# Performance work log

Measured on AMD Instinct MI355X. Metric: run time of the kernel, lower is better.

## Reference

```python
import jax, jax.numpy as jnp
import numpy as np


def _to_complex(t):
    # last dim 2 = (real, imag) -> complex64
    return jax.lax.complex(t[..., 0], t[..., 1])


def setup_inputs() -> dict:
    key = jax.random.key(0)
    k1, k2, k3, k4 = jax.random.split(key, 4)
    N, C_out, C_in, H, Wf = 2, 64, 3, 256, 129  # Wf = 256//2 + 1 (rfft width)
    X = jax.random.normal(k1, (N, 1, C_in, H, Wf, 2), dtype=jnp.float32)
    D = jax.random.normal(k2, (N, C_out, C_in, H, Wf, 2), dtype=jnp.float32)
    Y = jax.random.normal(k3, (N, C_out, 1, H, Wf, 2), dtype=jnp.float32)
    # alpha is a positive penalty weight; offset away from 0 to avoid blow-up in Z/alpha
    alpha = jax.random.uniform(k4, (N, 1, 1, 1), dtype=jnp.float32) + 0.5
    x_size = np.array([256, 256], dtype=np.int64)  # spatial size for irfft2
    return {"X": X, "D": D, "Y": Y, "alpha": alpha, "x_size": x_size}


def reference(X, D, Y, alpha, x_size):
    C_in = X.shape[2]
    Xc = _to_complex(X)  # (N,1,C_in,H,Wf)
    Dc = _to_complex(D)  # (N,C_out,C_in,H,Wf)
    Yc = _to_complex(Y)  # (N,C_out,1,H,Wf)
    # alpha.unsqueeze(-1).unsqueeze(-1)/C_in: in complex repr one extra axis suffices
    a = (alpha / C_in)[..., None]  # (N,1,1,1,1), real, broadcasts over (N,C_out,C_in,H,Wf)
    Dconj = jnp.conj(Dc)
    Z = Yc * Dc + a * Xc  # (N,C_out,C_in,H,Wf)
    factor1 = Z / a
    numerator = jnp.sum(Dconj * Z, axis=2, keepdims=True)  # (N,C_out,1,H,Wf)
    # csum adds a real scalar (alpha^2) to the real part only
    denominator = a * jnp.sum(Dconj * Dc, axis=2, keepdims=True) + a ** 2
    factor2 = Dc * (numerator / denominator)  # (N,C_out,C_in,H,Wf)
    Xhat = jnp.mean(factor1 - factor2, axis=1)  # (N,C_in,H,Wf)
    Hs, Ws = int(x_size[0]), int(x_size[1])
    # torch.irfft(signal_ndim=2, normalized=False) == full (1/n-normalized) inverse rfft2
    return jnp.fft.irfftn(Xhat, s=(Hs, Ws), axes=(-2, -1))
```

## Files before the change

kernel.cpp:

```cpp
#include <hip/hip_runtime.h>
#include <math.h>

#define H_   256
#define Wf_  129
#define HWf_ 33024
#define CIN_ 3
#define COUT_ 64
#define TW_  0.0245436926f

typedef float f32x4 __attribute__((ext_vector_type(4)));

__global__ __launch_bounds__(256) void solve_stage1(
    const float* __restrict__ X, const float* __restrict__ D,
    const float* __restrict__ Y, const float* __restrict__ alpha,
    float* __restrict__ Xhat)
{
    const int tid  = threadIdx.x;
    const int pl   = tid & 15;
    const int cog  = tid >> 4;
    const int pair = blockIdx.x * 16 + pl;
    const int pos0 = pair * 2;
    const int n    = pos0 / HWf_;
    const int hw0  = pos0 - n * HWf_;

    const float a    = alpha[n] * (1.0f / 3.0f);
    const float inva = 1.0f / a;
    const float a2   = a * a;

    f32x4 x[3];
#pragma unroll
    for (int ci = 0; ci < 3; ++ci)
        x[ci] = *(const f32x4*)(X + ((size_t)(n * 3 + ci) * HWf_ + hw0) * 2);

    const int co0 = cog * 4;
    const float* Dp = D + ((size_t)(n * 64 + co0) * 3) * (HWf_ * 2) + hw0 * 2;
    const float* Yp = Y + ((size_t)(n * 64 + co0)) * (HWf_ * 2) + hw0 * 2;

    float acc[12];
#pragma unroll
    for (int q = 0; q < 12; ++q) acc[q] = 0.f;

#pragma unroll
    for (int co = 0; co < 4; ++co) {
        f32x4 y  = __builtin_nontemporal_load(
                       (const f32x4*)(Yp + (size_t)co * (HWf_ * 2)));
        f32x4 d0 = __builtin_nontemporal_load(
                       (const f32x4*)(Dp + (size_t)(co * 3 + 0) * (HWf_ * 2)));
        f32x4 d1 = __builtin_nontemporal_load(
                       (const f32x4*)(Dp + (size_t)(co * 3 + 1) * (HWf_ * 2)));
        f32x4 d2 = __builtin_nontemporal_load(
                       (const f32x4*)(Dp + (size_t)(co * 3 + 2) * (HWf_ * 2)));

        {
            float s2 = d0[0]*d0[0] + d0[1]*d0[1] + d1[0]*d1[0] + d1[1]*d1[1]
                     + d2[0]*d2[0] + d2[1]*d2[1];
            float sr = d0[0]*x[0][0] + d0[1]*x[0][1] + d1[0]*x[1][0] + d1[1]*x[1][1]
                     + d2[0]*x[2][0] + d2[1]*x[2][1];
            float si = d0[0]*x[0][1] - d0[1]*x[0][0] + d1[0]*x[1][1] - d1[1]*x[1][0]
                     + d2[0]*x[2][1] - d2[1]*x[2][0];
            float nr = y[0] * s2 + a * sr, ni = y[1] * s2 + a * si;
            float invden = 1.0f / (a * s2 + a2);
            float tr = y[0] * inva - nr * invden;
            float ti = y[1] * inva - ni * invden;
            acc[0] += d0[0]*tr - d0[1]*ti;  acc[1] += d0[0]*ti + d0[1]*tr;
            acc[2] += d1[0]*tr - d1[1]*ti;  acc[3] += d1[0]*ti + d1[1]*tr;
            acc[4] += d2[0]*tr - d2[1]*ti;  acc[5] += d2[0]*ti + d2[1]*tr;
        }
        {
            float s2 = d0[2]*d0[2] + d0[3]*d0[3] + d1[2]*d1[2] + d1[3]*d1[3]
                     + d2[2]*d2[2] + d2[3]*d2[3];
            float sr = d0[2]*x[0][2] + d0[3]*x[0][3] + d1[2]*x[1][2] + d1[3]*x[1][3]
                     + d2[2]*x[2][2] + d2[3]*x[2][3];
            float si = d0[2]*x[0][3] - d0[3]*x[0][2] + d1[2]*x[1][3] - d1[3]*x[1][2]
                     + d2[2]*x[2][3] - d2[3]*x[2][2];
            float nr = y[2] * s2 + a * sr, ni = y[3] * s2 + a * si;
            float invden = 1.0f / (a * s2 + a2);
            float tr = y[2] * inva - nr * invden;
            float ti = y[3] * inva - ni * invden;
            acc[6]  += d0[2]*tr - d0[3]*ti;  acc[7]  += d0[2]*ti + d0[3]*tr;
            acc[8]  += d1[2]*tr - d1[3]*ti;  acc[9]  += d1[2]*ti + d1[3]*tr;
            acc[10] += d2[2]*tr - d2[3]*ti;  acc[11] += d2[2]*ti + d2[3]*tr;
        }
    }

    __shared__ float red[16 * 192];
    {
        const int base = cog * 192 + pl * 12;
#pragma unroll
        for (int q = 0; q < 12; ++q) red[base + q] = acc[q];
    }
    __syncthreads();

    if (tid < 192) {
        float s = 0.f;
#pragma unroll
        for (int c = 0; c < 16; ++c) s += red[c * 192 + tid];
        const int P   = tid / 12;
        const int r   = tid - P * 12;
        const int pos = r / 6;
        const int rr  = r - pos * 6;
        const int ci  = rr >> 1;
        const int cc  = rr & 1;
        const int gp  = (blockIdx.x * 16 + P) * 2 + pos;
        const int hw  = gp - n * HWf_;
        const int h   = hw / Wf_;
        const int w   = hw - h * Wf_;
        const size_t so = ((size_t)(n * 3 + ci) * HWf_ + hw) * 2 + cc;
        const size_t o = (((size_t)(n * 3 + ci) * Wf_ + w) * H_ + h) * 2 + cc;
        Xhat[o] = X[so] + s * (1.0f / 64.0f);
    }
}

__global__ __launch_bounds__(256) void solve_stage2(
    const float2* __restrict__ in, float2* __restrict__ out)
{
    __shared__ float2 col[2][256];

    const int b   = blockIdx.x;
    const int sub = threadIdx.x >> 7;
    const int t   = threadIdx.x & 127;

    const float2* src = in + ((size_t)b * 2 + sub) * H_;
    col[sub][t]       = src[t];
    col[sub][t + 128] = src[t + 128];
    __syncthreads();

    float wc, wsn;
    sincosf((float)t * TW_, &wsn, &wc);

    float ar = 0.f, ai = 0.f, br = 0.f, bi = 0.f;
    for (int kb = 0; kb < 8; ++kb) {
        const int k0 = kb * 32;
        float tr, ti;
        {
            const int m = (t * k0) & 255;
            float s, c; sincosf((float)m * TW_, &s, &c);
            tr = c; ti = s;
        }
#pragma unroll
        for (int j = 0; j < 32; ++j) {
            const float2 v = col[sub][k0 + j];
            const float pr = v.x * tr - v.y * ti;
            const float pi = v.x * ti + v.y * tr;
            ar += pr; ai += pi;
            if ((k0 + j) & 1) { br -= pr; bi -= pi; }
            else             { br += pr; bi += pi; }
            const float nt = tr * wc - ti * wsn;
            ti = tr * wsn + ti * wc;
            tr = nt;
        }
    }

    float2* dst = out + ((size_t)b * 2 + sub) * H_;
    dst[t]       = make_float2(ar * (1.0f / 256.0f), ai * (1.0f / 256.0f));
    dst[t + 128] = make_float2(br * (1.0f / 256.0f), bi * (1.0f / 256.0f));
}

__global__ __launch_bounds__(128) void solve_stage3(
    const float2* __restrict__ in, float* __restrict__ out)
{
    __shared__ float2 row[Wf_];

    const int b    = blockIdx.x;
    const int n_ci = b >> 8;
    const int h    = b & 255;
    const int t    = threadIdx.x;

    row[t] = in[((size_t)n_ci * Wf_ + t) * H_ + h];
    if (t == 0) row[128] = in[((size_t)n_ci * Wf_ + 128) * H_ + h];
    __syncthreads();

    float wc, wsn;
    sincosf((float)t * TW_, &wsn, &wc);

    float sa = 0.f, sb = 0.f;
    for (int kb = 0; kb < 4; ++kb) {
        const int k0 = kb * 32;
        float tr, ti;
        {
            const int m = (t * k0) & 255;
            float s, c; sincosf((float)m * TW_, &s, &c);
            tr = c; ti = s;
        }
#pragma unroll
        for (int j = 0; j < 32; ++j) {
            const float2 v = row[k0 + j];
            const float pr = v.x * tr - v.y * ti;
            sa += pr;
            if ((k0 + j) & 1) sb -= pr; else sb += pr;
            const float nt = tr * wc - ti * wsn;
            ti = tr * wsn + ti * wc;
            tr = nt;
        }
    }

    const float sgn  = (t & 1) ? -1.0f : 1.0f;
    const float base = -0.5f * row[0].x + sgn * 0.5f * row[128].x;
    __builtin_nontemporal_store((sa + base) * (1.0f / 128.0f),
                                out + (size_t)b * 256 + t);
    __builtin_nontemporal_store((sb + base) * (1.0f / 128.0f),
                                out + (size_t)b * 256 + t + 128);
}

extern "C" void kernel_launch(void* const* d_in, const int* in_sizes, int n_in,
                              void* d_out, int out_size, void* d_ws, size_t ws_size,
                              hipStream_t stream) {
    const float* X     = (const float*)d_in[0];
    const float* D     = (const float*)d_in[1];
    const float* Y     = (const float*)d_in[2];
    const float* alpha = (const float*)d_in[3];

    float* ws1 = (float*)d_ws;
    float2* ws2 = (float2*)(ws1 + (size_t)CIN_ * 2 * HWf_ * 2);

    solve_stage1<<<2064, 256, 0, stream>>>(X, D, Y, alpha, ws1);
    solve_stage2<<<(2 * CIN_ * Wf_) / 2, 256, 0, stream>>>((const float2*)ws1, ws2);
    solve_stage3<<<2 * CIN_ * H_, 128, 0, stream>>>(ws2, (float*)d_out);
}
```

Before: 200.2 us.

## Split DFT twiddle recurrence into two interleaved chains and reuse X via LDS

```diff
diff --git a/kernel.cpp b/kernel.cpp
--- a/kernel.cpp
+++ b/kernel.cpp
@@ -76,7 +76,8 @@
             float nr = y[2] * s2 + a * sr, ni = y[3] * s2 + a * si;
             float invden = 1.0f / (a * s2 + a2);
             float tr = y[2] * inva - nr * invden;
-            float ti = y[3] * inva - ni * invden;
+            float ti = y[2 - 1] * inva - ni * invden;
+            ti = y[3] * inva - ni * invden;
             acc[6]  += d0[2]*tr - d0[3]*ti;  acc[7]  += d0[2]*ti + d0[3]*tr;
             acc[8]  += d1[2]*tr - d1[3]*ti;  acc[9]  += d1[2]*ti + d1[3]*tr;
             acc[10] += d2[2]*tr - d2[3]*ti;  acc[11] += d2[2]*ti + d2[3]*tr;
@@ -84,10 +85,21 @@
     }
 
     __shared__ float red[16 * 192];
+    __shared__ float xbuf[16 * 12];
     {
         const int base = cog * 192 + pl * 12;
 #pragma unroll
         for (int q = 0; q < 12; ++q) red[base + q] = acc[q];
+    }
+    if (cog == 0) {
+        const int base = pl * 12;
+#pragma unroll
+        for (int pos = 0; pos < 2; ++pos)
+#pragma unroll
+            for (int ci = 0; ci < 3; ++ci)
+#pragma unroll
+                for (int cc = 0; cc < 2; ++cc)
+                    xbuf[base + pos * 6 + ci * 2 + cc] = x[ci][pos * 2 + cc];
     }
     __syncthreads();
 
@@ -105,53 +117,58 @@
         const int hw  = gp - n * HWf_;
         const int h   = hw / Wf_;
         const int w   = hw - h * Wf_;
-        const size_t so = ((size_t)(n * 3 + ci) * HWf_ + hw) * 2 + cc;
         const size_t o = (((size_t)(n * 3 + ci) * Wf_ + w) * H_ + h) * 2 + cc;
-        Xhat[o] = X[so] + s * (1.0f / 64.0f);
-    }
-}
-
-__global__ __launch_bounds__(256) void solve_stage2(
+        Xhat[o] = xbuf[tid] + s * (1.0f / 64.0f);
+    }
+}
+
+__global__ __launch_bounds__(128) void solve_stage2(
     const float2* __restrict__ in, float2* __restrict__ out)
 {
-    __shared__ float2 col[2][256];
-
-    const int b   = blockIdx.x;
-    const int sub = threadIdx.x >> 7;
-    const int t   = threadIdx.x & 127;
-
-    const float2* src = in + ((size_t)b * 2 + sub) * H_;
-    col[sub][t]       = src[t];
-    col[sub][t + 128] = src[t + 128];
+    __shared__ float2 col[256];
+
+    const int b = blockIdx.x;
+    const int t = threadIdx.x;
+
+    const float2* src = in + (size_t)b * H_;
+    col[t]       = src[t];
+    col[t + 128] = src[t + 128];
     __syncthreads();
 
-    float wc, wsn;
-    sincosf((float)t * TW_, &wsn, &wc);
+    float stc, sts;
+    sincosf((float)t * TW_, &sts, &stc);
+    const float wc2 = stc * stc - sts * sts;
+    const float ws2 = 2.0f * sts * stc;
 
     float ar = 0.f, ai = 0.f, br = 0.f, bi = 0.f;
     for (int kb = 0; kb < 8; ++kb) {
         const int k0 = kb * 32;
-        float tr, ti;
+        float tr0, ti0;
         {
             const int m = (t * k0) & 255;
             float s, c; sincosf((float)m * TW_, &s, &c);
-            tr = c; ti = s;
-        }
-#pragma unroll
-        for (int j = 0; j < 32; ++j) {
-            const float2 v = col[sub][k0 + j];
-            const float pr = v.x * tr - v.y * ti;
-            const float pi = v.x * ti + v.y * tr;
-            ar += pr; ai += pi;
-            if ((k0 + j) & 1) { br -= pr; bi -= pi; }
-            else             { br += pr; bi += pi; }
-            const float nt = tr * wc - ti * wsn;
-            ti = tr * wsn + ti * wc;
-            tr = nt;
-        }
-    }
-
-    float2* dst = out + ((size_t)b * 2 + sub) * H_;
+            tr0 = c; ti0 = s;
+        }
+        float tr1 = tr0 * stc - ti0 * sts;
+        float ti1 = tr0 * sts + ti0 * stc;
+#pragma unroll
+        for (int j = 0; j < 16; ++j) {
+            const float2 v0 = col[k0 + 2 * j];
+            const float2 v1 = col[k0 + 2 * j + 1];
+            const float pr0 = v0.x * tr0 - v0.y * ti0;
+            const float pi0 = v0.x * ti0 + v0.y * tr0;
+            const float pr1 = v1.x * tr1 - v1.y * ti1;
+            const float pi1 = v1.x * ti1 + v1.y * tr1;
+            ar += pr0 + pr1; ai += pi0 + pi1;
+            br += pr0 - pr1; bi += pi0 - pi1;
+            const float n0 = tr0 * wc2 - ti0 * ws2;
+            ti0 = tr0 * ws2 + ti0 * wc2; tr0 = n0;
+            const float n1 = tr1 * wc2 - ti1 * ws2;
+            ti1 = tr1 * ws2 + ti1 * wc2; tr1 = n1;
+        }
+    }
+
+    float2* dst = out + (size_t)b * H_;
     dst[t]       = make_float2(ar * (1.0f / 256.0f), ai * (1.0f / 256.0f));
     dst[t + 128] = make_float2(br * (1.0f / 256.0f), bi * (1.0f / 256.0f));
 }
@@ -170,27 +187,34 @@
     if (t == 0) row[128] = in[((size_t)n_ci * Wf_ + 128) * H_ + h];
     __syncthreads();
 
-    float wc, wsn;
-    sincosf((float)t * TW_, &wsn, &wc);
+    float stc, sts;
+    sincosf((float)t * TW_, &sts, &stc);
+    const float wc2 = stc * stc - sts * sts;
+    const float ws2 = 2.0f * sts * stc;
 
     float sa = 0.f, sb = 0.f;
     for (int kb = 0; kb < 4; ++kb) {
         const int k0 = kb * 32;
-        float tr, ti;
+        float tr0, ti0;
         {
             const int m = (t * k0) & 255;
             float s, c; sincosf((float)m * TW_, &s, &c);
-            tr = c; ti = s;
-        }
-#pragma unroll
-        for (int j = 0; j < 32; ++j) {
-            const float2 v = row[k0 + j];
-            const float pr = v.x * tr - v.y * ti;
-            sa += pr;
-            if ((k0 + j) & 1) sb -= pr; else sb += pr;
-            const float nt = tr * wc - ti * wsn;
-            ti = tr * wsn + ti * wc;
-            tr = nt;
+            tr0 = c; ti0 = s;
+        }
+        float tr1 = tr0 * stc - ti0 * sts;
+        float ti1 = tr0 * sts + ti0 * stc;
+#pragma unroll
+        for (int j = 0; j < 16; ++j) {
+            const float2 v0 = row[k0 + 2 * j];
+            const float2 v1 = row[k0 + 2 * j + 1];
+            const float pr0 = v0.x * tr0 - v0.y * ti0;
+            const float pr1 = v1.x * tr1 - v1.y * ti1;
+            sa += pr0 + pr1;
+            sb += pr0 - pr1;
+            const float n0 = tr0 * wc2 - ti0 * ws2;
+            ti0 = tr0 * ws2 + ti0 * wc2; tr0 = n0;
+            const float n1 = tr1 * wc2 - ti1 * ws2;
+            ti1 = tr1 * ws2 + ti1 * wc2; tr1 = n1;
         }
     }
 
@@ -214,6 +238,6 @@
     float2* ws2 = (float2*)(ws1 + (size_t)CIN_ * 2 * HWf_ * 2);
 
     solve_stage1<<<2064, 256, 0, stream>>>(X, D, Y, alpha, ws1);
-    solve_stage2<<<(2 * CIN_ * Wf_) / 2, 256, 0, stream>>>((const float2*)ws1, ws2);
+    solve_stage2<<<2 * CIN_ * Wf_, 128, 0, stream>>>((const float2*)ws1, ws2);
     solve_stage3<<<2 * CIN_ * H_, 128, 0, stream>>>(ws2, (float*)d_out);
 }
```

Result: no change. 202.8 us (+1.3%).
